# Optimization experiments

Measured on AMD Instinct MI355X. Metric: run time of the kernel, lower is better.

Reference implementation:

```python
import jax, jax.numpy as jnp
import numpy as np

B, N0, NCLS = 8, 1024, 40
SPACING, SIGMA_FACTOR = 2.0, 1.0
BLOCKS = [[64, 64], [128, 128], [256, 1024]]
POOL_SIZES = [256, 64, 1]
FC1, FC2 = 512, 256
# 3x3x3 kernel translation grid (27-point support, hard-coded in ConvLayer)
GRID = jnp.asarray(np.array([[i, j, k] for i in (-1, 0, 1) for j in (-1, 0, 1) for k in (-1, 0, 1)], dtype=np.float32))  # [27,3]


def pcnn_conv(pc, feat, W, b, sigma):
    """Extension-operator point convolution.
    pc [B,N,3], feat [B,N,Cin], W [27,Cin,Cout], b [Cout].
    out[b,i,o] = relu( (1/N) * sum_l sum_j exp(-||p_i - p_j + t_l||^2/(2 ks^2)) f[b,j] @ W[l] + b )
    """
    ks = SIGMA_FACTOR * sigma
    trans = SPACING * sigma * GRID                      # [27,3]
    inv = 1.0 / (2.0 * ks * ks)
    diff = pc[:, :, None, :] - pc[:, None, :, :]        # [B,N,N,3]
    d2 = jnp.sum(diff * diff, -1)                       # [B,N,N]
    n = pc.shape[1]

    def body(acc, wt):
        t, Wl = wt                                      # t [3], Wl [Cin,Cout]
        # ||diff + t||^2 = d2 + 2 diff.t + |t|^2
        e = jnp.exp(-(d2 + 2.0 * jnp.einsum('bijd,d->bij', diff, t) + jnp.dot(t, t)) * inv)
        s = jnp.einsum('bij,bjc->bic', e, feat)         # Gaussian-weighted gather
        return acc + jnp.einsum('bic,co->bio', s, Wl), None

    out0 = jnp.zeros((pc.shape[0], n, W.shape[2]), feat.dtype)
    out, _ = jax.lax.scan(body, out0, (trans, W))
    return jax.nn.relu(out / n + b)


def fps(pts, m):
    """Farthest point sampling. pts [N,3] -> indices [m]."""
    d = jnp.sum((pts - pts[0]) ** 2, -1)
    idxs = jnp.zeros((m,), jnp.int32)

    def body(i, state):
        idxs, d = state
        nxt = jnp.argmax(d).astype(jnp.int32)
        idxs = idxs.at[i].set(nxt)
        d = jnp.minimum(d, jnp.sum((pts - pts[nxt]) ** 2, -1))
        return idxs, d

    idxs, _ = jax.lax.fori_loop(1, m, body, (idxs, d))
    return idxs


def pool(pc, feat, m):
    """FPS subsample to m centers, max-pool features over nearest-center clusters."""
    idx = jax.vmap(lambda p: fps(p, m))(pc)                      # [B,m]
    centers = jnp.take_along_axis(pc, idx[..., None], axis=1)    # [B,m,3]
    dist = jnp.sum((pc[:, :, None, :] - centers[:, None, :, :]) ** 2, -1)  # [B,N,m]
    assign = jnp.argmin(dist, -1)                                # [B,N]
    pooled = jax.vmap(lambda f, a: jax.ops.segment_max(f, a, num_segments=m))(feat, assign)
    return centers, pooled


def bn(x, g, b):
    mu = jnp.mean(x, 0)
    v = jnp.var(x, 0)
    return g * (x - mu) * jax.lax.rsqrt(v + 1e-5) + b


def setup_inputs() -> dict:
    key = jax.random.key(0)
    ks = jax.random.split(key, 24)
    inp = {"pc": jax.random.normal(ks[0], (B, 3, N0), jnp.float32)}
    chans = [4, 64, 64, 128, 128, 256, 1024]
    for i, (ci, co) in enumerate(zip(chans[:-1], chans[1:])):
        inp[f"w_c{i}"] = jax.random.normal(ks[1 + i], (27, ci, co), jnp.float32) * 0.05
        inp[f"b_c{i}"] = jnp.zeros((co,), jnp.float32)
    inp["w_fc1"] = jax.random.normal(ks[10], (1024, FC1), jnp.float32) * 0.03
    inp["g_fc1"] = jnp.ones((FC1,), jnp.float32)
    inp["be_fc1"] = jnp.zeros((FC1,), jnp.float32)
    inp["w_fc2"] = jax.random.normal(ks[11], (FC1, FC2), jnp.float32) * 0.05
    inp["g_fc2"] = jnp.ones((FC2,), jnp.float32)
    inp["be_fc2"] = jnp.zeros((FC2,), jnp.float32)
    inp["w_fc3"] = jax.random.normal(ks[12], (FC2, NCLS), jnp.float32) * 0.05
    inp["b_fc3"] = jnp.zeros((NCLS,), jnp.float32)
    return inp


def reference(pc, w_c0, b_c0, w_c1, b_c1, w_c2, b_c2, w_c3, b_c3, w_c4, b_c4, w_c5, b_c5,
              w_fc1, g_fc1, be_fc1, w_fc2, g_fc2, be_fc2, w_fc3, b_fc3):
    pts = jnp.transpose(pc, (0, 2, 1))                           # [B,N,3]
    b_, n0, _ = pts.shape
    feat = jnp.concatenate([pts, jnp.ones((b_, n0, 1), pts.dtype)], -1)  # [B,N,4]
    sigma = 1.0 / float(np.sqrt(n0))  # faithfully uses initial N for all blocks
    ws = [(w_c0, b_c0), (w_c1, b_c1), (w_c2, b_c2), (w_c3, b_c3), (w_c4, b_c4), (w_c5, b_c5)]
    idx = 0
    cur = pts
    for bi, block in enumerate(BLOCKS):
        for _ in block:
            W, bb = ws[idx]
            feat = pcnn_conv(cur, feat, W, bb, sigma)
            idx += 1
        cur, feat = pool(cur, feat, POOL_SIZES[bi])
    x = feat.reshape(b_, -1)                                     # [B,1024]
    x = jax.nn.relu(bn(x @ w_fc1, g_fc1, be_fc1))
    x = jax.nn.relu(bn(x @ w_fc2, g_fc2, be_fc2))
    return x @ w_fc3 + b_fc3
```

## Files before the change

kernel.cpp:

```cpp
#include <hip/hip_runtime.h>
#include <cstdint>
#include <cstddef>
#include <cmath>

constexpr int B = 8;
constexpr int N0 = 1024;
constexpr int CAP = 64;
using u16 = unsigned short;

typedef __bf16 bf16x8 __attribute__((ext_vector_type(8)));
typedef float f32x4 __attribute__((ext_vector_type(4)));

__device__ inline u16 f2bf(float x) {
  unsigned u = __float_as_uint(x);
  return (u16)((u + 0x7fffu + ((u >> 16) & 1u)) >> 16);
}
__device__ inline float bf2f(u16 h) { return __uint_as_float(((unsigned)h) << 16); }
__device__ inline int swk(int row, int k) {
  return ((((k >> 3) ^ ((row >> 2) & 3)) << 3) | (k & 7));
}

__global__ __launch_bounds__(256) void k_prep(const float* __restrict__ pc,
                                              float* __restrict__ pts,
                                              float* __restrict__ feat0) {
  int idx = blockIdx.x * blockDim.x + threadIdx.x;
  if (idx >= B * N0) return;
  int b = idx / N0, i = idx - b * N0;
  float x = pc[(b * 3 + 0) * N0 + i];
  float y = pc[(b * 3 + 1) * N0 + i];
  float z = pc[(b * 3 + 2) * N0 + i];
  pts[idx * 3 + 0] = x; pts[idx * 3 + 1] = y; pts[idx * 3 + 2] = z;
  feat0[idx * 4 + 0] = x; feat0[idx * 4 + 1] = y; feat0[idx * 4 + 2] = z; feat0[idx * 4 + 3] = 1.0f;
}

__global__ __launch_bounds__(256) void k_pairs(const float* __restrict__ pts,
                                               int* __restrict__ pidx, int* __restrict__ pcnt,
                                               int N) {
  const int r = blockIdx.x * 4 + (threadIdx.x >> 6);
  const int lane = threadIdx.x & 63;
  const int b = r / N;
  const float px = pts[(size_t)r * 3 + 0];
  const float py = pts[(size_t)r * 3 + 1];
  const float pz = pts[(size_t)r * 3 + 2];
  int* row = pidx + (size_t)r * CAP;
  int base = 0;
  for (int j0 = 0; j0 < N; j0 += 64) {
    int j = j0 + lane;
    float dx = px - pts[((size_t)b * N + j) * 3 + 0];
    float dy = py - pts[((size_t)b * N + j) * 3 + 1];
    float dz = pz - pts[((size_t)b * N + j) * 3 + 2];
    float d2 = dx * dx + dy * dy + dz * dz;
    bool keep = d2 <= 0.1228f;
    unsigned long long mk = __ballot(keep);
    int pos = __popcll(mk & ((1ull << lane) - 1ull));
    if (keep) { int s = base + pos; if (s < CAP) row[s] = j; }
    base += __popcll(mk);
  }
  if (lane == 0) pcnt[r] = base < CAP ? base : CAP;
}

__global__ void k_econtract(const float* __restrict__ pts, const float* __restrict__ feat,
                            const int* __restrict__ pidx, const int* __restrict__ pcnt,
                            u16* __restrict__ Shi, u16* __restrict__ Slo,
                            int N, int Cin, int K, int Kpad, int mbase) {
  const int g = mbase + blockIdx.x;
  const int b = g / N;
  const int t = threadIdx.x;
  const bool cact = t < Cin;
  const float px = pts[(size_t)g * 3 + 0];
  const float py = pts[(size_t)g * 3 + 1];
  const float pz = pts[(size_t)g * 3 + 2];
  float acc[27];
#pragma unroll
  for (int l = 0; l < 27; ++l) acc[l] = 0.f;
  const int n = pcnt[g];
  const int* row = pidx + (size_t)g * CAP;
  for (int p = 0; p < n; ++p) {
    int j = row[p];
    size_t jb = (size_t)b * N + j;
    float dx = px - pts[jb * 3 + 0];
    float dy = py - pts[jb * 3 + 1];
    float dz = pz - pts[jb * 3 + 2];
    float d2 = dx * dx + dy * dy + dz * dz;
    float base_ = __expf(-512.f * d2);
    float gxv[3] = {__expf(64.f * dx - 2.f), 1.f, __expf(-64.f * dx - 2.f)};
    float gyv[3] = {__expf(64.f * dy - 2.f), 1.f, __expf(-64.f * dy - 2.f)};
    float gzv[3] = {__expf(64.f * dz - 2.f), 1.f, __expf(-64.f * dz - 2.f)};
    float fv = cact ? feat[jb * Cin + t] : 0.f;
#pragma unroll
    for (int a = 0; a < 3; ++a) {
      float ba = base_ * gxv[a];
#pragma unroll
      for (int b2 = 0; b2 < 3; ++b2) {
        float bab = ba * gyv[b2];
#pragma unroll
        for (int c2 = 0; c2 < 3; ++c2) {
          int l = a * 9 + b2 * 3 + c2;
          acc[l] = fmaf(bab * gzv[c2], fv, acc[l]);
        }
      }
    }
  }
  size_t rowo = (size_t)blockIdx.x * Kpad;
  if (cact) {
#pragma unroll
    for (int l = 0; l < 27; ++l) {
      float v = acc[l];
      u16 h = f2bf(v);
      u16 lo = f2bf(v - bf2f(h));
      Shi[rowo + (size_t)l * Cin + t] = h;
      Slo[rowo + (size_t)l * Cin + t] = lo;
    }
  }
  if (Kpad > K && t >= Cin && t < Cin + (Kpad - K)) {
    size_t po = rowo + K + (t - Cin);
    Shi[po] = 0; Slo[po] = 0;
  }
}

__global__ __launch_bounds__(512) void k_gemm_mfma(const u16* __restrict__ Shi,
                                                   const u16* __restrict__ Slo,
                                                   const float* __restrict__ W,
                                                   const float* __restrict__ bias,
                                                   float* __restrict__ out,
                                                   float* __restrict__ P,
                                                   int K, int Kpad, int Cout, float scale,
                                                   int mcur) {
  __shared__ u16 As[2][2][32][40];
  __shared__ u16 Bs[2][2][64][40];
  __shared__ float xch[4][64][8];
  const int t = threadIdx.x;
  const int h = t >> 8;
  const int tl = t & 255;
  const int nb = blockIdx.x * 64;
  const int m0 = blockIdx.y * 32;
  const int l = t & 63, w = t >> 6;
  const int ks = w >> 2, wq = w & 3;
  const int wm = (wq >> 1) * 16, wn = (wq & 1) * 32;
  const int la = l & 15, lg = l >> 4;
  const int ntiles = Kpad >> 6;
  const int KZ = gridDim.z, z = blockIdx.z;
  const int q = ntiles / KZ, r = ntiles % KZ;
  const int t0 = z * q + (z < r ? z : r);
  const int cnt = q + (z < r ? 1 : 0);
  const int ar = tl >> 3, ak = (tl & 7) * 4;
  const size_t aOff = (size_t)(m0 + ar) * Kpad + h * 32 + ak;
  const int aw = swk(ar, ak);
  const int kp = (tl >> 4) * 2, n4 = (tl & 15) * 4;
  f32x4 acc0 = {0.f, 0.f, 0.f, 0.f}, acc1 = {0.f, 0.f, 0.f, 0.f};

  for (int kt = 0; kt < cnt; ++kt) {
    const int k0 = (t0 + kt) * 64;
    *(ushort4*)&As[h][0][ar][aw] = *(const ushort4*)(Shi + aOff + k0);
    *(ushort4*)&As[h][1][ar][aw] = *(const ushort4*)(Slo + aOff + k0);
    {
      int gk0 = k0 + h * 32 + kp;
      float4 b0 = make_float4(0.f, 0.f, 0.f, 0.f), b1 = b0;
      if (gk0 < K) b0 = *(const float4*)(W + (size_t)gk0 * Cout + nb + n4);
      if (gk0 + 1 < K) b1 = *(const float4*)(W + (size_t)(gk0 + 1) * Cout + nb + n4);
      float v0[4] = {b0.x, b0.y, b0.z, b0.w};
      float v1[4] = {b1.x, b1.y, b1.z, b1.w};
#pragma unroll
      for (int e = 0; e < 4; ++e) {
        int n = n4 + e;
        int kw = swk(n, kp);
        u16 h0 = f2bf(v0[e]);
        u16 l0 = f2bf(v0[e] - bf2f(h0));
        u16 h1 = f2bf(v1[e]);
        u16 l1 = f2bf(v1[e] - bf2f(h1));
        *(unsigned*)&Bs[h][0][n][kw] = (unsigned)h0 | ((unsigned)h1 << 16);
        *(unsigned*)&Bs[h][1][n][kw] = (unsigned)l0 | ((unsigned)l1 << 16);
      }
    }
    __syncthreads();
    bf16x8 ah = *(const bf16x8*)&As[ks][0][wm + la][swk(wm + la, lg * 8)];
    bf16x8 al = *(const bf16x8*)&As[ks][1][wm + la][swk(wm + la, lg * 8)];
    bf16x8 bh0 = *(const bf16x8*)&Bs[ks][0][wn + la][swk(wn + la, lg * 8)];
    bf16x8 bl0 = *(const bf16x8*)&Bs[ks][1][wn + la][swk(wn + la, lg * 8)];
    bf16x8 bh1 = *(const bf16x8*)&Bs[ks][0][wn + 16 + la][swk(wn + 16 + la, lg * 8)];
    bf16x8 bl1 = *(const bf16x8*)&Bs[ks][1][wn + 16 + la][swk(wn + 16 + la, lg * 8)];
    acc0 = __builtin_amdgcn_mfma_f32_16x16x32_bf16(ah, bh0, acc0, 0, 0, 0);
    acc1 = __builtin_amdgcn_mfma_f32_16x16x32_bf16(ah, bh1, acc1, 0, 0, 0);
    acc0 = __builtin_amdgcn_mfma_f32_16x16x32_bf16(al, bh0, acc0, 0, 0, 0);
    acc1 = __builtin_amdgcn_mfma_f32_16x16x32_bf16(al, bh1, acc1, 0, 0, 0);
    acc0 = __builtin_amdgcn_mfma_f32_16x16x32_bf16(ah, bl0, acc0, 0, 0, 0);
    acc1 = __builtin_amdgcn_mfma_f32_16x16x32_bf16(ah, bl1, acc1, 0, 0, 0);
    __syncthreads();
  }
  if (w >= 4) {
#pragma unroll
    for (int r2 = 0; r2 < 4; ++r2) { xch[wq][l][r2] = acc0[r2]; xch[wq][l][r2 + 4] = acc1[r2]; }
  }
  __syncthreads();
  if (w < 4) {
#pragma unroll
    for (int r2 = 0; r2 < 4; ++r2) { acc0[r2] += xch[wq][l][r2]; acc1[r2] += xch[wq][l][r2 + 4]; }
    if (gridDim.z == 1) {
#pragma unroll
      for (int r2 = 0; r2 < 4; ++r2) {
        int gm = m0 + wm + lg * 4 + r2;
        int gn0 = nb + wn + la;
        out[(size_t)gm * Cout + gn0] = fmaxf(fmaf(acc0[r2], scale, bias[gn0]), 0.f);
        int gn1 = gn0 + 16;
        out[(size_t)gm * Cout + gn1] = fmaxf(fmaf(acc1[r2], scale, bias[gn1]), 0.f);
      }
    } else {
      float* Pz = P + (size_t)z * mcur * Cout;
#pragma unroll
      for (int r2 = 0; r2 < 4; ++r2) {
        int gm = m0 + wm + lg * 4 + r2;
        int gn0 = nb + wn + la;
        Pz[(size_t)gm * Cout + gn0] = acc0[r2];
        Pz[(size_t)gm * Cout + gn0 + 16] = acc1[r2];
      }
    }
  }
}

__global__ __launch_bounds__(256) void k_reduce(const float* __restrict__ P,
                                                const float* __restrict__ bias,
                                                float* __restrict__ out,
                                                int n4, int Cout, int KZ, float scale,
                                                int stride ) {
  int i = blockIdx.x * 256 + threadIdx.x;
  if (i >= n4) return;
  float4 s = *(const float4*)(P + (size_t)i * 4);
  for (int z = 1; z < KZ; ++z) {
    float4 v = *(const float4*)(P + (size_t)z * stride + (size_t)i * 4);
    s.x += v.x; s.y += v.y; s.z += v.z; s.w += v.w;
  }
  int c = (i * 4) % Cout;
  float4 bb = *(const float4*)(bias + c);
  float4 o;
  o.x = fmaxf(fmaf(s.x, scale, bb.x), 0.f);
  o.y = fmaxf(fmaf(s.y, scale, bb.y), 0.f);
  o.z = fmaxf(fmaf(s.z, scale, bb.z), 0.f);
  o.w = fmaxf(fmaf(s.w, scale, bb.w), 0.f);
  *(float4*)(out + (size_t)i * 4) = o;
}

template <int CTRL>
__device__ __forceinline__ void dppmax(unsigned& hi, unsigned& lo) {
  unsigned thi = (unsigned)__builtin_amdgcn_update_dpp(0, (int)hi, CTRL, 0xF, 0xF, true);
  unsigned tlo = (unsigned)__builtin_amdgcn_update_dpp(0, (int)lo, CTRL, 0xF, 0xF, true);
  bool g = (thi > hi) || (thi == hi && tlo > lo);
  hi = g ? thi : hi;
  lo = g ? tlo : lo;
}

template <int NQ> __device__ __forceinline__ float treesel(const float* q, int qsel);
template <> __device__ __forceinline__ float treesel<1>(const float* q, int) { return q[0]; }
template <> __device__ __forceinline__ float treesel<4>(const float* q, int qsel) {
  bool e0 = qsel & 1, e1 = qsel & 2;
  float a0 = e0 ? q[1] : q[0], a1 = e0 ? q[3] : q[2];
  return e1 ? a1 : a0;
}

template <int N>
__global__ __launch_bounds__(256) void k_fps4(const float* __restrict__ pts,
                                              float* __restrict__ centers, int m,
                                              unsigned* __restrict__ pooled, int pcount) {
  constexpr int NQ = N / 256;
  __shared__ unsigned rhi[4], rlo[4];
  __shared__ float cshare[3];
  const int b = blockIdx.x;
  const int t = threadIdx.x, lane = t & 63, w = t >> 6;
  const float* P = pts + (size_t)b * N * 3;
  float qx[NQ], qy[NQ], qz[NQ], d[NQ];
  float x0 = P[0], y0 = P[1], z0 = P[2];
  float lbest = -1.f; int lj = 0;
#pragma unroll
  for (int q = 0; q < NQ; ++q) {
    int j = t + q * 256;
    float x = P[j * 3 + 0], y = P[j * 3 + 1], z = P[j * 3 + 2];
    qx[q] = x; qy[q] = y; qz[q] = z;
    float dx = __fsub_rn(x, x0), dy = __fsub_rn(y, y0), dz = __fsub_rn(z, z0);
    float dd = __fadd_rn(__fadd_rn(__fmul_rn(dx, dx), __fmul_rn(dy, dy)), __fmul_rn(dz, dz));
    d[q] = dd;
    bool g = dd > lbest; lbest = g ? dd : lbest; lj = g ? j : lj;
  }
  if (t == 0) {
    centers[(size_t)b * m * 3 + 0] = x0;
    centers[(size_t)b * m * 3 + 1] = y0;
    centers[(size_t)b * m * 3 + 2] = z0;
  }
  for (int it = 1; it < m; ++it) {
    unsigned hi = __float_as_uint(lbest), lo = ~(unsigned)lj;
    dppmax<0xB1>(hi, lo);
    dppmax<0x4E>(hi, lo);
    dppmax<0x141>(hi, lo);
    dppmax<0x140>(hi, lo);
    dppmax<0x142>(hi, lo);
    dppmax<0x143>(hi, lo);
    if (lane == 63) { rhi[w] = hi; rlo[w] = lo; }
    __syncthreads();
    unsigned bh = rhi[0], bl = rlo[0];
#pragma unroll
    for (int u = 1; u < 4; ++u) {
      unsigned ohu = rhi[u], olu = rlo[u];
      bool g = (ohu > bh) || (ohu == bh && olu > bl);
      bh = g ? ohu : bh;
      bl = g ? olu : bl;
    }
    int wj = (int)(~bl);
    if (t == (wj & 255)) {
      int qs = wj >> 8;
      float sx = treesel<NQ>(qx, qs);
      float sy = treesel<NQ>(qy, qs);
      float sz = treesel<NQ>(qz, qs);
      cshare[0] = sx; cshare[1] = sy; cshare[2] = sz;
      centers[((size_t)b * m + it) * 3 + 0] = sx;
      centers[((size_t)b * m + it) * 3 + 1] = sy;
      centers[((size_t)b * m + it) * 3 + 2] = sz;
    }
    __syncthreads();
    float cx = cshare[0], cy = cshare[1], cz = cshare[2];
    lbest = -1.f; lj = 0;
#pragma unroll
    for (int q = 0; q < NQ; ++q) {
      int j = t + q * 256;
      float dx = __fsub_rn(qx[q], cx), dy = __fsub_rn(qy[q], cy), dz = __fsub_rn(qz[q], cz);
      float nd = __fadd_rn(__fadd_rn(__fmul_rn(dx, dx), __fmul_rn(dy, dy)), __fmul_rn(dz, dz));
      float dn = fminf(d[q], nd);
      d[q] = dn;
      bool g = dn > lbest; lbest = g ? dn : lbest; lj = g ? j : lj;
    }
  }
  unsigned* pp = pooled + (size_t)b * pcount;
  for (int i = t; i < pcount; i += 256) pp[i] = 0xFFFFFFFFu;
}

__global__ __launch_bounds__(256) void k_center0(const float* __restrict__ pts,
                                                 float* __restrict__ centers,
                                                 int* __restrict__ assign,
                                                 unsigned* __restrict__ pooled) {
  const int b = blockIdx.x, t = threadIdx.x;
  if (t < 3) centers[b * 3 + t] = pts[(size_t)b * 64 * 3 + t];
  if (t < 64) assign[b * 64 + t] = 0;
  unsigned* pp = pooled + (size_t)b * 1024;
  for (int i = t; i < 1024; i += 256) pp[i] = 0xFFFFFFFFu;
}

__global__ __launch_bounds__(256) void k_assign(const float* __restrict__ pts,
                                                const float* __restrict__ centers,
                                                int* __restrict__ assign, int N, int m) {
  __shared__ float cs[256 * 3];
  const int t = threadIdx.x;
  const int idx = blockIdx.x * 256 + t;
  const int b = (blockIdx.x * 256) / N;
  for (int i = t; i < m * 3; i += 256) cs[i] = centers[(size_t)b * m * 3 + i];
  __syncthreads();
  float px = pts[(size_t)idx * 3 + 0], py = pts[(size_t)idx * 3 + 1], pz = pts[(size_t)idx * 3 + 2];
  float best = 3.4e38f; int bk = 0;
  for (int k = 0; k < m; ++k) {
    float dx = __fsub_rn(px, cs[k * 3 + 0]);
    float dy = __fsub_rn(py, cs[k * 3 + 1]);
    float dz = __fsub_rn(pz, cs[k * 3 + 2]);
    float dd = __fadd_rn(__fadd_rn(__fmul_rn(dx, dx), __fmul_rn(dy, dy)), __fmul_rn(dz, dz));
    if (dd < best) { best = dd; bk = k; }
  }
  assign[idx] = bk;
}

__global__ __launch_bounds__(256) void k_segmax(const float* __restrict__ feat,
                                                const int* __restrict__ assign,
                                                float* __restrict__ pooled,
                                                int N, int m, int C) {
  int idx = blockIdx.x * blockDim.x + threadIdx.x;
  if (idx >= B * N * C) return;
  int b = idx / (N * C);
  int r = idx - b * N * C;
  int i = r / C;
  int c = r - i * C;
  int a = assign[b * N + i];
  atomicMax((int*)&pooled[((size_t)b * m + a) * C + c], __float_as_int(feat[idx]));
}

template <int K, int COUT, bool BNR>
__global__ __launch_bounds__(256) void k_fc(const float* __restrict__ x,
                                            const float* __restrict__ w,
                                            const float* __restrict__ g,
                                            const float* __restrict__ be,
                                            float* __restrict__ out) {
  __shared__ float ys[8][33];
  int t = threadIdx.x;
  int n = t >> 5, cl = t & 31;
  int c = blockIdx.x * 32 + cl;
  float acc = 0.f;
  if (c < COUT) {
    const float* xr = x + n * K;
    float a0 = 0.f, a1 = 0.f, a2 = 0.f, a3 = 0.f;
    for (int k = 0; k < K; k += 4) {
      a0 = fmaf(xr[k + 0], w[(size_t)(k + 0) * COUT + c], a0);
      a1 = fmaf(xr[k + 1], w[(size_t)(k + 1) * COUT + c], a1);
      a2 = fmaf(xr[k + 2], w[(size_t)(k + 2) * COUT + c], a2);
      a3 = fmaf(xr[k + 3], w[(size_t)(k + 3) * COUT + c], a3);
    }
    acc = (a0 + a1) + (a2 + a3);
  }
  ys[n][cl] = acc;
  __syncthreads();
  if (c >= COUT) return;
  if (BNR) {
    float mu = 0.f;
#pragma unroll
    for (int q = 0; q < 8; ++q) mu += ys[q][cl];
    mu *= 0.125f;
    float var = 0.f;
#pragma unroll
    for (int q = 0; q < 8; ++q) { float dv = ys[q][cl] - mu; var = fmaf(dv, dv, var); }
    var *= 0.125f;
    float rs = 1.f / sqrtf(var + 1e-5f);
    float v = g[c] * (acc - mu) * rs + be[c];
    out[n * COUT + c] = fmaxf(v, 0.f);
  } else {
    out[n * COUT + c] = acc + be[c];
  }
}

extern "C" void kernel_launch(void* const* d_in, const int* in_sizes, int n_in,
                              void* d_out, int out_size, void* d_ws, size_t ws_size,
                              hipStream_t stream) {
  (void)in_sizes; (void)n_in; (void)out_size;
  const float* pc = (const float*)d_in[0];
  const float* Wc[6]; const float* bc[6];
  for (int l = 0; l < 6; ++l) { Wc[l] = (const float*)d_in[1 + 2 * l]; bc[l] = (const float*)d_in[2 + 2 * l]; }
  const float* w1 = (const float*)d_in[13];
  const float* g1 = (const float*)d_in[14];
  const float* be1 = (const float*)d_in[15];
  const float* w2 = (const float*)d_in[16];
  const float* g2 = (const float*)d_in[17];
  const float* be2 = (const float*)d_in[18];
  const float* w3 = (const float*)d_in[19];
  const float* b3 = (const float*)d_in[20];

  float* ws = (float*)d_ws;
  size_t o = 0;
  auto A = [&](size_t n) { size_t r = o; o += (n + 63) & ~(size_t)63; return r; };
  const size_t PTS0 = A((size_t)B * 1024 * 3);
  const size_t PTS1 = A((size_t)B * 256 * 3);
  const size_t PTS2 = A((size_t)B * 64 * 3);
  const size_t PTS3 = A((size_t)B * 3);
  const size_t F0  = A((size_t)B * 1024 * 4);
  const size_t FB1 = A((size_t)B * 1024 * 64);
  const size_t FB2 = A((size_t)B * 1024 * 64);
  const size_t FB3 = A((size_t)B * 256 * 64);
  const size_t FB4 = A((size_t)B * 256 * 128);
  const size_t FB5 = A((size_t)B * 256 * 128);
  const size_t FB6 = A((size_t)B * 64 * 128);
  const size_t FB7 = A((size_t)B * 64 * 256);
  const size_t FB8 = A((size_t)B * 64 * 1024);
  const size_t FB9 = A((size_t)B * 1024);
  const size_t ASSIGN = A((size_t)B * 1024);
  const size_t Y1 = A((size_t)8 * 512);
  const size_t Y2 = A((size_t)8 * 256);
  const size_t PIDX = A((size_t)B * 1024 * CAP);
  const size_t PCNT = A((size_t)B * 1024);
  const size_t dynB = o * sizeof(float);

  int* pidx = (int*)(ws + PIDX);
  int* pcnt = (int*)(ws + PCNT);

  k_prep<<<dim3((B * N0 + 255) / 256), dim3(256), 0, stream>>>(pc, ws + PTS0, ws + F0);

  auto conv = [&](size_t ptsOff, size_t finOff, size_t foutOff, int Npts, int Cin, int Cout,
                  const float* W, const float* bias) {
    const int M = B * Npts;
    const int K = 27 * Cin;
    const int Kpad = (K + 63) & ~63;
    const size_t availB = (ws_size > dynB) ? ws_size - dynB : 0;
    size_t pResB = availB / 4;
    if (pResB > (size_t)13 << 20) pResB = (size_t)13 << 20;
    const size_t sByte = availB - pResB;
    long mc = (long)(sByte / ((size_t)Kpad * 4)) & ~31L;
    int Mc = (int)((mc < (long)M) ? mc : (long)M);
    if (Mc < 32) Mc = 32;
    u16* Shi = (u16*)((char*)d_ws + dynB);
    u16* Slo = Shi + (size_t)Mc * Kpad;
    float* P = (float*)(Shi + (size_t)2 * Mc * Kpad);
    const int mch = (M + Mc - 1) / Mc;
    const float scale = 1.f / (float)Npts;
    const int blk = (Cin <= 64) ? 64 : Cin;
    const int ntiles = Kpad >> 6;
    for (int mcb = 0; mcb < mch; ++mcb) {
      const int mb0 = mcb * Mc;
      const int mcur = ((M - mb0) < Mc) ? (M - mb0) : Mc;
      k_econtract<<<dim3(mcur), dim3(blk), 0, stream>>>(ws + ptsOff, ws + finOff, pidx, pcnt,
                                                        Shi, Slo, Npts, Cin, K, Kpad, mb0);
      const int gx = Cout / 64, gy = mcur / 32;
      int kz = 1024 / (gx * gy);
      if (kz < 1) kz = 1;
      if (kz > ntiles) kz = ntiles;
      if (kz > 16) kz = 16;
      long pcap = (long)(pResB / ((size_t)mcur * Cout * 4));
      if ((long)kz > pcap) kz = (pcap < 1) ? 1 : (int)pcap;
      float* outp = ws + foutOff + (size_t)mb0 * Cout;
      k_gemm_mfma<<<dim3(gx, gy, kz), dim3(512), 0, stream>>>(
          Shi, Slo, W, bias, outp, P, K, Kpad, Cout, scale, mcur);
      if (kz > 1) {
        int n4 = mcur * Cout / 4;
        k_reduce<<<dim3((n4 + 255) / 256), dim3(256), 0, stream>>>(
            P, bias, outp, n4, Cout, kz, scale, mcur * Cout);
      }
    }
  };

  k_pairs<<<dim3(B * 1024 / 4), dim3(256), 0, stream>>>(ws + PTS0, pidx, pcnt, 1024);
  conv(PTS0, F0, FB1, 1024, 4, 64, Wc[0], bc[0]);
  conv(PTS0, FB1, FB2, 1024, 64, 64, Wc[1], bc[1]);
  k_fps4<1024><<<dim3(B), dim3(256), 0, stream>>>(ws + PTS0, ws + PTS1, 256,
                                                  (unsigned*)(ws + FB3), 256 * 64);
  k_assign<<<dim3(B * 1024 / 256), dim3(256), 0, stream>>>(ws + PTS0, ws + PTS1, (int*)(ws + ASSIGN), 1024, 256);
  k_segmax<<<dim3((B * 1024 * 64 + 255) / 256), dim3(256), 0, stream>>>(ws + FB2, (int*)(ws + ASSIGN), ws + FB3, 1024, 256, 64);
  k_pairs<<<dim3(B * 256 / 4), dim3(256), 0, stream>>>(ws + PTS1, pidx, pcnt, 256);
  conv(PTS1, FB3, FB4, 256, 64, 128, Wc[2], bc[2]);
  conv(PTS1, FB4, FB5, 256, 128, 128, Wc[3], bc[3]);
  k_fps4<256><<<dim3(B), dim3(256), 0, stream>>>(ws + PTS1, ws + PTS2, 64,
                                                 (unsigned*)(ws + FB6), 64 * 128);
  k_assign<<<dim3(B * 256 / 256), dim3(256), 0, stream>>>(ws + PTS1, ws + PTS2, (int*)(ws + ASSIGN), 256, 64);
  k_segmax<<<dim3((B * 256 * 128 + 255) / 256), dim3(256), 0, stream>>>(ws + FB5, (int*)(ws + ASSIGN), ws + FB6, 256, 64, 128);
  k_pairs<<<dim3(B * 64 / 4), dim3(256), 0, stream>>>(ws + PTS2, pidx, pcnt, 64);
  conv(PTS2, FB6, FB7, 64, 128, 256, Wc[4], bc[4]);
  conv(PTS2, FB7, FB8, 64, 256, 1024, Wc[5], bc[5]);
  k_center0<<<dim3(B), dim3(256), 0, stream>>>(ws + PTS2, ws + PTS3, (int*)(ws + ASSIGN),
                                               (unsigned*)(ws + FB9));
  k_segmax<<<dim3((B * 64 * 1024 + 255) / 256), dim3(256), 0, stream>>>(ws + FB8, (int*)(ws + ASSIGN), ws + FB9, 64, 1, 1024);
  k_fc<1024, 512, true><<<dim3(512 / 32), dim3(256), 0, stream>>>(ws + FB9, w1, g1, be1, ws + Y1);
  k_fc<512, 256, true><<<dim3(256 / 32), dim3(256), 0, stream>>>(ws + Y1, w2, g2, be2, ws + Y2);
  k_fc<256, 40, false><<<dim3(2), dim3(256), 0, stream>>>(ws + Y2, w3, nullptr, b3, (float*)d_out);
}
```

Before: 501.0 us.

## Cut FPS to one barrier per iteration and retune GEMM LDS swizzle

The farthest-point-sampling loop now reduces only the float distance with DPP, finds the winning lane by ballot, and has that lane publish value, index and coordinates into a double-buffered shared slot. This removes the second barrier and the 64-bit packed compare from each of the sequential iterations. Points are reassigned to threads contiguously (t*NQ+q) so that the smallest-index tie-break still matches. Separately, the GEMM's LDS XOR swizzle now also mixes in row bit 4, aimed at reducing bank conflicts.

Result: slower. 528.4 us (+5.5%).

```diff
diff --git a/kernel.cpp b/kernel.cpp
--- a/kernel.cpp
+++ b/kernel.cpp
@@ -16,8 +16,9 @@
   return (u16)((u + 0x7fffu + ((u >> 16) & 1u)) >> 16);
 }
 __device__ inline float bf2f(u16 h) { return __uint_as_float(((unsigned)h) << 16); }
-__device__ inline int swk(int row, int k) {
-  return ((((k >> 3) ^ ((row >> 2) & 3)) << 3) | (k & 7));
+__device__ inline int swk2(int row, int k) {
+  int s = (((row >> 2) ^ (row >> 4)) & 3);
+  return ((((k >> 3) ^ s) << 3) | (k & 7));
 }
 
 __global__ __launch_bounds__(256) void k_prep(const float* __restrict__ pc,
@@ -145,7 +146,7 @@
   const int cnt = q + (z < r ? 1 : 0);
   const int ar = tl >> 3, ak = (tl & 7) * 4;
   const size_t aOff = (size_t)(m0 + ar) * Kpad + h * 32 + ak;
-  const int aw = swk(ar, ak);
+  const int aw = swk2(ar, ak);
   const int kp = (tl >> 4) * 2, n4 = (tl & 15) * 4;
   f32x4 acc0 = {0.f, 0.f, 0.f, 0.f}, acc1 = {0.f, 0.f, 0.f, 0.f};
 
@@ -163,7 +164,7 @@
 #pragma unroll
       for (int e = 0; e < 4; ++e) {
         int n = n4 + e;
-        int kw = swk(n, kp);
+        int kw = swk2(n, kp);
         u16 h0 = f2bf(v0[e]);
         u16 l0 = f2bf(v0[e] - bf2f(h0));
         u16 h1 = f2bf(v1[e]);
@@ -173,12 +174,12 @@
       }
     }
     __syncthreads();
-    bf16x8 ah = *(const bf16x8*)&As[ks][0][wm + la][swk(wm + la, lg * 8)];
-    bf16x8 al = *(const bf16x8*)&As[ks][1][wm + la][swk(wm + la, lg * 8)];
-    bf16x8 bh0 = *(const bf16x8*)&Bs[ks][0][wn + la][swk(wn + la, lg * 8)];
-    bf16x8 bl0 = *(const bf16x8*)&Bs[ks][1][wn + la][swk(wn + la, lg * 8)];
-    bf16x8 bh1 = *(const bf16x8*)&Bs[ks][0][wn + 16 + la][swk(wn + 16 + la, lg * 8)];
-    bf16x8 bl1 = *(const bf16x8*)&Bs[ks][1][wn + 16 + la][swk(wn + 16 + la, lg * 8)];
+    bf16x8 ah = *(const bf16x8*)&As[ks][0][wm + la][swk2(wm + la, lg * 8)];
+    bf16x8 al = *(const bf16x8*)&As[ks][1][wm + la][swk2(wm + la, lg * 8)];
+    bf16x8 bh0 = *(const bf16x8*)&Bs[ks][0][wn + la][swk2(wn + la, lg * 8)];
+    bf16x8 bl0 = *(const bf16x8*)&Bs[ks][1][wn + la][swk2(wn + la, lg * 8)];
+    bf16x8 bh1 = *(const bf16x8*)&Bs[ks][0][wn + 16 + la][swk2(wn + 16 + la, lg * 8)];
+    bf16x8 bl1 = *(const bf16x8*)&Bs[ks][1][wn + 16 + la][swk2(wn + 16 + la, lg * 8)];
     acc0 = __builtin_amdgcn_mfma_f32_16x16x32_bf16(ah, bh0, acc0, 0, 0, 0);
     acc1 = __builtin_amdgcn_mfma_f32_16x16x32_bf16(ah, bh1, acc1, 0, 0, 0);
     acc0 = __builtin_amdgcn_mfma_f32_16x16x32_bf16(al, bh0, acc0, 0, 0, 0);
@@ -221,7 +222,7 @@
                                                 const float* __restrict__ bias,
                                                 float* __restrict__ out,
                                                 int n4, int Cout, int KZ, float scale,
-                                                int stride ) {
+                                                int stride) {
   int i = blockIdx.x * 256 + threadIdx.x;
   if (i >= n4) return;
   float4 s = *(const float4*)(P + (size_t)i * 4);
@@ -240,12 +241,9 @@
 }
 
 template <int CTRL>
-__device__ __forceinline__ void dppmax(unsigned& hi, unsigned& lo) {
-  unsigned thi = (unsigned)__builtin_amdgcn_update_dpp(0, (int)hi, CTRL, 0xF, 0xF, true);
-  unsigned tlo = (unsigned)__builtin_amdgcn_update_dpp(0, (int)lo, CTRL, 0xF, 0xF, true);
-  bool g = (thi > hi) || (thi == hi && tlo > lo);
-  hi = g ? thi : hi;
-  lo = g ? tlo : lo;
+__device__ __forceinline__ float dppmaxf(float v) {
+  int o = __builtin_amdgcn_update_dpp(0, __float_as_int(v), CTRL, 0xF, 0xF, true);
+  return fmaxf(v, __int_as_float(o));
 }
 
 template <int NQ> __device__ __forceinline__ float treesel(const float* q, int qsel);
@@ -261,8 +259,7 @@
                                               float* __restrict__ centers, int m,
                                               unsigned* __restrict__ pooled, int pcount) {
   constexpr int NQ = N / 256;
-  __shared__ unsigned rhi[4], rlo[4];
-  __shared__ float cshare[3];
+  __shared__ float ent[2][4][5];
   const int b = blockIdx.x;
   const int t = threadIdx.x, lane = t & 63, w = t >> 6;
   const float* P = pts + (size_t)b * N * 3;
@@ -271,13 +268,13 @@
   float lbest = -1.f; int lj = 0;
 #pragma unroll
   for (int q = 0; q < NQ; ++q) {
-    int j = t + q * 256;
+    int j = t * NQ + q;
     float x = P[j * 3 + 0], y = P[j * 3 + 1], z = P[j * 3 + 2];
     qx[q] = x; qy[q] = y; qz[q] = z;
     float dx = __fsub_rn(x, x0), dy = __fsub_rn(y, y0), dz = __fsub_rn(z, z0);
     float dd = __fadd_rn(__fadd_rn(__fmul_rn(dx, dx), __fmul_rn(dy, dy)), __fmul_rn(dz, dz));
     d[q] = dd;
-    bool g = dd > lbest; lbest = g ? dd : lbest; lj = g ? j : lj;
+    bool g = dd > lbest; lbest = g ? dd : lbest; lj = g ? q : lj;
   }
   if (t == 0) {
     centers[(size_t)b * m * 3 + 0] = x0;
@@ -285,45 +282,48 @@
     centers[(size_t)b * m * 3 + 2] = z0;
   }
   for (int it = 1; it < m; ++it) {
-    unsigned hi = __float_as_uint(lbest), lo = ~(unsigned)lj;
-    dppmax<0xB1>(hi, lo);
-    dppmax<0x4E>(hi, lo);
-    dppmax<0x141>(hi, lo);
-    dppmax<0x140>(hi, lo);
-    dppmax<0x142>(hi, lo);
-    dppmax<0x143>(hi, lo);
-    if (lane == 63) { rhi[w] = hi; rlo[w] = lo; }
+    const int eb = it & 1;
+    float v = lbest;
+    v = dppmaxf<0xB1>(v);
+    v = dppmaxf<0x4E>(v);
+    v = dppmaxf<0x141>(v);
+    v = dppmaxf<0x140>(v);
+    v = dppmaxf<0x142>(v);
+    v = dppmaxf<0x143>(v);
+    float wmax = __uint_as_float((unsigned)__builtin_amdgcn_readlane(__float_as_int(v), 63));
+    unsigned long long mask = __ballot(lbest == wmax);
+    int fl = __ffsll((long long)mask) - 1;
+    if (lane == fl) {
+      float* e = ent[eb][w];
+      e[0] = wmax;
+      e[1] = __int_as_float(t * NQ + lj);
+      e[2] = treesel<NQ>(qx, lj);
+      e[3] = treesel<NQ>(qy, lj);
+      e[4] = treesel<NQ>(qz, lj);
+    }
     __syncthreads();
-    unsigned bh = rhi[0], bl = rlo[0];
+    float bm = ent[eb][0][0]; int bj = __float_as_int(ent[eb][0][1]);
+    float cx = ent[eb][0][2], cy = ent[eb][0][3], cz = ent[eb][0][4];
 #pragma unroll
     for (int u = 1; u < 4; ++u) {
-      unsigned ohu = rhi[u], olu = rlo[u];
-      bool g = (ohu > bh) || (ohu == bh && olu > bl);
-      bh = g ? ohu : bh;
-      bl = g ? olu : bl;
-    }
-    int wj = (int)(~bl);
-    if (t == (wj & 255)) {
-      int qs = wj >> 8;
-      float sx = treesel<NQ>(qx, qs);
-      float sy = treesel<NQ>(qy, qs);
-      float sz = treesel<NQ>(qz, qs);
-      cshare[0] = sx; cshare[1] = sy; cshare[2] = sz;
-      centers[((size_t)b * m + it) * 3 + 0] = sx;
-      centers[((size_t)b * m + it) * 3 + 1] = sy;
-      centers[((size_t)b * m + it) * 3 + 2] = sz;
-    }
-    __syncthreads();
-    float cx = cshare[0], cy = cshare[1], cz = cshare[2];
+      float em = ent[eb][u][0]; int ej = __float_as_int(ent[eb][u][1]);
+      bool g = (em > bm) || (em == bm && ej < bj);
+      bm = g ? em : bm; bj = g ? ej : bj;
+      cx = g ? ent[eb][u][2] : cx; cy = g ? ent[eb][u][3] : cy; cz = g ? ent[eb][u][4] : cz;
+    }
+    if (t == 0) {
+      centers[((size_t)b * m + it) * 3 + 0] = cx;
+      centers[((size_t)b * m + it) * 3 + 1] = cy;
+      centers[((size_t)b * m + it) * 3 + 2] = cz;
+    }
     lbest = -1.f; lj = 0;
 #pragma unroll
     for (int q = 0; q < NQ; ++q) {
-      int j = t + q * 256;
       float dx = __fsub_rn(qx[q], cx), dy = __fsub_rn(qy[q], cy), dz = __fsub_rn(qz[q], cz);
       float nd = __fadd_rn(__fadd_rn(__fmul_rn(dx, dx), __fmul_rn(dy, dy)), __fmul_rn(dz, dz));
       float dn = fminf(d[q], nd);
       d[q] = dn;
-      bool g = dn > lbest; lbest = g ? dn : lbest; lj = g ? j : lj;
+      bool g = dn > lbest; lbest = g ? dn : lbest; lj = g ? q : lj;
     }
   }
   unsigned* pp = pooled + (size_t)b * pcount;
```
